# Kernel tuning notes

Hardware: AMD Instinct MI355X
Metric: run time of the kernel (lower is better)

Reference implementation:

```python
import jax, jax.numpy as jnp
import numpy as np

HIDDEN = 4096
N_HEADS = 32
N_KV_HEADS = 8
HEAD_DIM = HIDDEN // N_HEADS  # 128
N_GROUPS = N_HEADS // N_KV_HEADS  # 4
ROPE_THETA = 10000.0


def setup_inputs() -> dict:
    key = jax.random.key(0)
    k1, k2, k3, k4, k5 = jax.random.split(key, 5)
    B, S = 2, 2048
    hidden_states = jax.random.normal(k1, (B, S, HIDDEN), dtype=jnp.float32)
    position_ids = jnp.arange(S, dtype=jnp.int64 if jax.config.jax_enable_x64 else jnp.int32)[None, :]
    scale = 0.02
    Wq = jax.random.normal(k2, (N_HEADS * HEAD_DIM, HIDDEN), dtype=jnp.float32) * scale
    Wk = jax.random.normal(k3, (N_KV_HEADS * HEAD_DIM, HIDDEN), dtype=jnp.float32) * scale
    Wv = jax.random.normal(k4, (N_KV_HEADS * HEAD_DIM, HIDDEN), dtype=jnp.float32) * scale
    Wo = jax.random.normal(k5, (HIDDEN, N_HEADS * HEAD_DIM), dtype=jnp.float32) * scale
    return {"hidden_states": hidden_states, "position_ids": position_ids,
            "Wq": Wq, "Wk": Wk, "Wv": Wv, "Wo": Wo}


def _rope_cos_sin(position_ids, dtype):
    # inv_freq: [HEAD_DIM/2]
    inv_freq = 1.0 / (ROPE_THETA ** (jnp.arange(0, HEAD_DIM, 2, dtype=jnp.float32) / HEAD_DIM))
    freqs = position_ids.astype(jnp.float32)[..., None] * inv_freq  # [1, S, D/2]
    emb = jnp.concatenate([freqs, freqs], axis=-1)                  # [1, S, D]
    return jnp.cos(emb).astype(dtype), jnp.sin(emb).astype(dtype)


def _rotate_half(x):
    x1, x2 = jnp.split(x, 2, axis=-1)
    return jnp.concatenate([-x2, x1], axis=-1)


def reference(hidden_states, position_ids, Wq, Wk, Wv, Wo):
    B, S, H = hidden_states.shape
    d = HEAD_DIM
    # projections -> [B, heads, S, d]
    q = (hidden_states @ Wq.T).reshape(B, S, N_HEADS, d).transpose(0, 2, 1, 3)
    k = (hidden_states @ Wk.T).reshape(B, S, N_KV_HEADS, d).transpose(0, 2, 1, 3)
    v = (hidden_states @ Wv.T).reshape(B, S, N_KV_HEADS, d).transpose(0, 2, 1, 3)
    cos, sin = _rope_cos_sin(position_ids, q.dtype)  # [1, S, d]
    cos, sin = cos[:, None], sin[:, None]            # [1, 1, S, d]
    q = q * cos + _rotate_half(q) * sin
    k = k * cos + _rotate_half(k) * sin
    # GQA: group query heads over shared kv heads (no explicit expand)
    qg = q.reshape(B, N_KV_HEADS, N_GROUPS, S, d)
    scores = jnp.einsum('bkgqd,bkld->bkgql', qg, k) / jnp.sqrt(jnp.asarray(d, q.dtype))
    w = jax.nn.softmax(scores, axis=-1)  # NOTE: no causal mask, matching source
    o = jnp.einsum('bkgql,bkld->bkgqd', w, v)        # [B, kvh, g, S, d]
    o = o.reshape(B, N_HEADS, S, d).transpose(0, 2, 1, 3).reshape(B, S, N_HEADS * d)
    return o @ Wo.T
```

## Files before the change

kernel.cpp:

```cpp
#include <hip/hip_runtime.h>
#include <math.h>

#define HIDDEN 4096
#define NH 32
#define NKV 8
#define HD 128
#define BBATCH 2
#define SEQ 2048
#define BS 4096
#define QKVD 6144

typedef __attribute__((ext_vector_type(8))) short short8;
typedef __attribute__((ext_vector_type(4))) float f32x4;
typedef __attribute__((ext_vector_type(4))) unsigned int uint4v;

__device__ __forceinline__ unsigned short f2bf(float f) {
  union { float f; unsigned int u; } v; v.f = f;
  unsigned int r = v.u + 0x7fffu + ((v.u >> 16) & 1u);
  return (unsigned short)(r >> 16);
}
__device__ __forceinline__ float bf2f(unsigned short u) {
  union { unsigned int u; float f; } v; v.u = ((unsigned int)u) << 16;
  return v.f;
}
__device__ __forceinline__ unsigned int cvtpk(float lo, float hi) {
  unsigned int r;
  asm("v_cvt_pk_bf16_f32 %0, %1, %2" : "=v"(r) : "v"(lo), "v"(hi));
  return r;
}

__device__ __forceinline__ void gload16(const unsigned short* g, unsigned short* l) {
  __builtin_amdgcn_global_load_lds((const __attribute__((address_space(1))) unsigned int*)(const void*)g,
                                   (__attribute__((address_space(3))) unsigned int*)(void*)l, 16, 0, 0);
}

__global__ void cast_all(const float* __restrict__ h, const float* __restrict__ q,
                         const float* __restrict__ k, const float* __restrict__ v,
                         const float* __restrict__ o,
                         unsigned short* hx, unsigned short* wq, unsigned short* wk,
                         unsigned short* wv, unsigned short* wo) {
  int b = blockIdx.x;
  const float* src; unsigned short* dst; int base;
  if (b < 16384)      { src = h; dst = hx; base = 0; }
  else if (b < 32768) { src = q; dst = wq; base = 16384; }
  else if (b < 36864) { src = k; dst = wk; base = 32768; }
  else if (b < 40960) { src = v; dst = wv; base = 36864; }
  else                { src = o; dst = wo; base = 40960; }
  size_t i = ((size_t)(b - base) * 256 + threadIdx.x) * 4;
  float4 f = *(const float4*)(src + i);
  ushort4 u;
  u.x = f2bf(f.x); u.y = f2bf(f.y); u.z = f2bf(f.z); u.w = f2bf(f.w);
  *(ushort4*)(dst + i) = u;
}

template<int OUT_F32>
__global__ __launch_bounds__(256) void gemm_bt128(const unsigned short* __restrict__ A,
                                                  const unsigned short* __restrict__ Bm,
                                                  void* __restrict__ Cc,
                                                  int M, int N, int K) {
  __shared__ unsigned short As[128 * 32];
  __shared__ unsigned short Bs[128 * 32];
  int t = threadIdx.x, lane = t & 63, wave = t >> 6;
  int lm = lane & 15, quad = lane >> 4;
  int wm = wave >> 1, wn = wave & 1;
  int m0 = blockIdx.y * 128, n0 = blockIdx.x * 128;
  int srow = t >> 2;
  int pcol = (((t & 3) ^ (srow & 3)) * 8);
  f32x4 acc[4][4] = {};
  const unsigned short* ag = A + (size_t)(m0 + srow) * K + pcol;
  const unsigned short* bg = Bm + (size_t)(n0 + srow) * K + pcol;
  unsigned short* asl = &As[(size_t)t * 8];
  unsigned short* bsl = &Bs[(size_t)t * 8];
  for (int k0 = 0; k0 < K; k0 += 32) {
    __syncthreads();
    gload16(ag + k0, asl);
    gload16(ag + (size_t)64 * K + k0, asl + 2048);
    gload16(bg + k0, bsl);
    gload16(bg + (size_t)64 * K + k0, bsl + 2048);
    __syncthreads();
    int xq = (quad ^ (lm & 3)) * 8;
    short8 af[4], bf[4];
#pragma unroll
    for (int mt = 0; mt < 4; mt++)
      af[mt] = *(const short8*)&As[(wm * 64 + mt * 16 + lm) * 32 + xq];
#pragma unroll
    for (int nt = 0; nt < 4; nt++)
      bf[nt] = *(const short8*)&Bs[(wn * 64 + nt * 16 + lm) * 32 + xq];
#pragma unroll
    for (int mt = 0; mt < 4; mt++)
#pragma unroll
      for (int nt = 0; nt < 4; nt++)
        acc[mt][nt] = __builtin_amdgcn_mfma_f32_16x16x32_bf16(af[mt], bf[nt], acc[mt][nt], 0, 0, 0);
  }
#pragma unroll
  for (int mt = 0; mt < 4; mt++)
#pragma unroll
    for (int nt = 0; nt < 4; nt++)
#pragma unroll
      for (int r = 0; r < 4; r++) {
        size_t row = m0 + wm * 64 + mt * 16 + quad * 4 + r;
        size_t col = n0 + wn * 64 + nt * 16 + lm;
        if (OUT_F32) ((float*)Cc)[row * N + col] = acc[mt][nt][r];
        else ((unsigned short*)Cc)[row * N + col] = f2bf(acc[mt][nt][r]);
      }
}

__global__ void build_rope_table(const int* __restrict__ pos, float2* __restrict__ cs) {
  int idx = blockIdx.x * blockDim.x + threadIdx.x;
  int j = idx & 63, s = idx >> 6;
  float p = (float)pos[s];
  float f = p * exp2f(-(float)j * (13.287712379549449f / 64.0f));
  cs[idx] = make_float2(cosf(f), sinf(f));
}

__global__ void rope_fused(unsigned short* __restrict__ x, const float2* __restrict__ cs) {
  int idx = blockIdx.x * blockDim.x + threadIdx.x;
  int j = idx & 63;
  int q6 = idx >> 6;
  int hh = q6 % 40;
  int row = q6 / 40;
  int s = row & (SEQ - 1);
  float2 t2 = cs[(s << 6) | j];
  unsigned short* ptr = x + (size_t)row * QKVD + hh * HD;
  float x1 = bf2f(ptr[j]), x2 = bf2f(ptr[j + 64]);
  ptr[j]      = f2bf(x1 * t2.x - x2 * t2.y);
  ptr[j + 64] = f2bf(x2 * t2.x + x1 * t2.y);
}

__global__ void transpose_v(const unsigned short* __restrict__ v, unsigned short* __restrict__ vt) {
  __shared__ unsigned short tile[64][72];
  int bx = blockIdx.x;
  int s0 = (bx & 31) * 64;
  int d0 = ((bx >> 5) & 1) * 64;
  int bk = bx >> 6;
  int b = bk >> 3, kv = bk & 7;
  int t = threadIdx.x;
  int rs = t >> 2, rc = (t & 3) * 16;
  const unsigned short* src = v + ((size_t)(b * SEQ + s0 + rs)) * QKVD + kv * HD + d0 + rc;
  *(uint4*)&tile[rs][rc]     = *(const uint4*)src;
  *(uint4*)&tile[rs][rc + 8] = *(const uint4*)(src + 8);
  __syncthreads();
  int wd = t >> 2, wc = (t & 3) * 16;
  short8 o0, o1;
#pragma unroll
  for (int e = 0; e < 8; e++) o0[e] = (short)tile[wc + e][wd];
#pragma unroll
  for (int e = 0; e < 8; e++) o1[e] = (short)tile[wc + 8 + e][wd];
  unsigned short* dst = vt + ((size_t)bk * HD + d0 + wd) * SEQ + s0 + wc;
  *(short8*)dst = o0;
  *(short8*)(dst + 8) = o1;
}

__global__ __launch_bounds__(256) void attn_kernel(const unsigned short* __restrict__ Q,
                                                   const unsigned short* __restrict__ Kb,
                                                   const unsigned short* __restrict__ Vt,
                                                   unsigned short* __restrict__ O) {
  __shared__ unsigned short Ksh[2 * 64 * 128];
  __shared__ unsigned short Vsh[2 * 128 * 64];
  int t = threadIdx.x, wave = t >> 6, lane = t & 63;
  int lm = lane & 15, quad = lane >> 4;
  int blk0 = blockIdx.x;
  int blk = (blk0 & 7) * 128 + (blk0 >> 3);
  int qt = blk & 15;
  int h = (blk >> 4) & 31;
  int b = blk >> 9;
  int kv = h >> 2;
  int qs0 = qt * 128 + wave * 32;
  const float c = 0.08838834764831845f * 1.4426950408889634f;

  short8 aq[2][4];
#pragma unroll
  for (int s = 0; s < 2; s++) {
    const unsigned short* qbase = Q + ((size_t)(b * SEQ + qs0 + s * 16 + lm)) * QKVD + h * HD;
#pragma unroll
    for (int kk = 0; kk < 4; kk++)
      aq[s][kk] = *(const short8*)(qbase + kk * 32 + quad * 8);
  }

  f32x4 acc[2][8] = {};
  float mrow[2] = {-1e30f, -1e30f};
  float lrow[2] = {0.f, 0.f};
  const unsigned short* kbase = Kb + (size_t)b * SEQ * QKVD + kv * HD;
  const unsigned short* vbase = Vt + ((size_t)(b * NKV + kv)) * HD * SEQ;

  int trow = t >> 4;
  int kchunk = (t & 15) ^ (trow & 7);
  const unsigned short* ksrc[4];
#pragma unroll
  for (int i = 0; i < 4; i++) {
    int srow = i * 16 + trow;
    int key = (srow & 0x20) | ((srow & 0x0C) << 1) | ((srow & 0x10) >> 2) | (srow & 3);
    ksrc[i] = kbase + (size_t)key * QKVD + kchunk * 8;
  }
  int vrow = t >> 3;
  int vchunk = (t & 7) ^ (vrow & 7);
  const unsigned short* vsrc[4];
#pragma unroll
  for (int i = 0; i < 4; i++)
    vsrc[i] = vbase + (size_t)(i * 32 + vrow) * SEQ + vchunk * 8;

  int xr8 = (lm & 7) * 8;

  {
    unsigned short* kd = Ksh + t * 8;
    unsigned short* vd = Vsh + t * 8;
#pragma unroll
    for (int i = 0; i < 4; i++) gload16(ksrc[i], kd + i * 2048);
#pragma unroll
    for (int i = 0; i < 4; i++) gload16(vsrc[i], vd + i * 2048);
#pragma unroll
    for (int i = 0; i < 4; i++) { ksrc[i] += 64 * QKVD; vsrc[i] += 64; }
  }
  asm volatile("s_waitcnt vmcnt(0)" ::: "memory");
  __syncthreads();

  int cur = 0;
  for (int it = 0; it < SEQ / 64; it++) {
    if (it < SEQ / 64 - 1) {
      unsigned short* kd = Ksh + (cur ^ 1) * 8192 + t * 8;
      unsigned short* vd = Vsh + (cur ^ 1) * 8192 + t * 8;
#pragma unroll
      for (int i = 0; i < 4; i++) gload16(ksrc[i], kd + i * 2048);
#pragma unroll
      for (int i = 0; i < 4; i++) gload16(vsrc[i], vd + i * 2048);
#pragma unroll
      for (int i = 0; i < 4; i++) { ksrc[i] += 64 * QKVD; vsrc[i] += 64; }
    }
    const unsigned short* kcur = Ksh + cur * 8192;
    const unsigned short* vcur = Vsh + cur * 8192;
    f32x4 sc[2][4] = {};
    __builtin_amdgcn_s_setprio(1);
#pragma unroll
    for (int kt = 0; kt < 4; kt++) {
#pragma unroll
      for (int kk = 0; kk < 4; kk++) {
        short8 bk = *(const short8*)&kcur[(kt * 16 + lm) * 128 + (((kk * 4 + quad) * 8) ^ xr8)];
        sc[0][kt] = __builtin_amdgcn_mfma_f32_16x16x32_bf16(bk, aq[0][kk], sc[0][kt], 0, 0, 0);
        sc[1][kt] = __builtin_amdgcn_mfma_f32_16x16x32_bf16(bk, aq[1][kk], sc[1][kt], 0, 0, 0);
      }
    }
    __builtin_amdgcn_s_setprio(0);
    union PW { uint4v w; short8 h; } pw[2][2];
#pragma unroll
    for (int s = 0; s < 2; s++) {
      float vmax = -1e30f;
#pragma unroll
      for (int kt = 0; kt < 4; kt++)
        vmax = fmaxf(vmax, fmaxf(fmaxf(sc[s][kt][0], sc[s][kt][1]),
                                 fmaxf(sc[s][kt][2], sc[s][kt][3])));
      vmax *= c;
      vmax = fmaxf(vmax, __shfl_xor(vmax, 16));
      vmax = fmaxf(vmax, __shfl_xor(vmax, 32));
      if (__any(vmax > mrow[s] + 8.0f)) {
        float nm = fmaxf(mrow[s], vmax);
        float alpha = __builtin_amdgcn_exp2f(mrow[s] - nm);
        mrow[s] = nm;
        lrow[s] *= alpha;
#pragma unroll
        for (int r = 0; r < 4; r++) {
          float ar = __shfl(alpha, quad * 4 + r);
#pragma unroll
          for (int tt = 0; tt < 8; tt++) acc[s][tt][r] *= ar;
        }
      }
      float nm = mrow[s];
      float rs = 0.f;
#pragma unroll
      for (int kt = 0; kt < 4; kt++) {
        float p0 = __builtin_amdgcn_exp2f(sc[s][kt][0] * c - nm);
        float p1 = __builtin_amdgcn_exp2f(sc[s][kt][1] * c - nm);
        float p2 = __builtin_amdgcn_exp2f(sc[s][kt][2] * c - nm);
        float p3 = __builtin_amdgcn_exp2f(sc[s][kt][3] * c - nm);
        rs += (p0 + p1) + (p2 + p3);
        pw[s][kt >> 1].w[(kt & 1) * 2 + 0] = cvtpk(p0, p1);
        pw[s][kt >> 1].w[(kt & 1) * 2 + 1] = cvtpk(p2, p3);
      }
      rs += __shfl_xor(rs, 16);
      rs += __shfl_xor(rs, 32);
      lrow[s] += rs;
    }
    __builtin_amdgcn_s_setprio(1);
#pragma unroll
    for (int g = 0; g < 2; g++) {
      short8 ap0 = pw[0][g].h;
      short8 ap1 = pw[1][g].h;
#pragma unroll
      for (int tt = 0; tt < 8; tt++) {
        short8 bv = *(const short8*)&vcur[(tt * 16 + lm) * 64 + (((g * 4 + quad) * 8) ^ xr8)];
        acc[0][tt] = __builtin_amdgcn_mfma_f32_16x16x32_bf16(ap0, bv, acc[0][tt], 0, 0, 0);
        acc[1][tt] = __builtin_amdgcn_mfma_f32_16x16x32_bf16(ap1, bv, acc[1][tt], 0, 0, 0);
      }
    }
    __builtin_amdgcn_s_setprio(0);
    asm volatile("s_waitcnt vmcnt(0)" ::: "memory");
    __syncthreads();
    cur ^= 1;
  }
#pragma unroll
  for (int s = 0; s < 2; s++) {
#pragma unroll
    for (int r = 0; r < 4; r++) {
      float lq = __shfl(lrow[s], quad * 4 + r);
      float inv = 1.0f / lq;
      int row = qs0 + s * 16 + quad * 4 + r;
      unsigned short* op = O + ((size_t)(b * SEQ + row)) * HIDDEN + h * HD;
#pragma unroll
      for (int tt = 0; tt < 8; tt++)
        op[tt * 16 + lm] = f2bf(acc[s][tt][r] * inv);
    }
  }
}

extern "C" void kernel_launch(void* const* d_in, const int* in_sizes, int n_in,
                              void* d_out, int out_size, void* d_ws, size_t ws_size,
                              hipStream_t stream) {
  const float* hidden = (const float*)d_in[0];
  const int*   pos    = (const int*)d_in[1];
  const float* Wq     = (const float*)d_in[2];
  const float* Wk     = (const float*)d_in[3];
  const float* Wv     = (const float*)d_in[4];
  const float* Wo     = (const float*)d_in[5];

  char* ws = (char*)d_ws;
  unsigned short* hx  = (unsigned short*)ws; ws += (size_t)BS * HIDDEN * 2;
  unsigned short* wq  = (unsigned short*)ws; ws += (size_t)HIDDEN * HIDDEN * 2;
  unsigned short* wk  = (unsigned short*)ws; ws += (size_t)1024 * HIDDEN * 2;
  unsigned short* wv  = (unsigned short*)ws; ws += (size_t)1024 * HIDDEN * 2;
  unsigned short* wo  = (unsigned short*)ws; ws += (size_t)HIDDEN * HIDDEN * 2;
  unsigned short* qkv = (unsigned short*)ws; ws += (size_t)BS * QKVD * 2;
  unsigned short* vt  = (unsigned short*)ws; ws += (size_t)BS * 1024 * 2;
  unsigned short* ob  = (unsigned short*)ws; ws += (size_t)BS * HIDDEN * 2;
  float2*         cs  = (float2*)ws;         ws += (size_t)SEQ * 64 * sizeof(float2);

  build_rope_table<<<512, 256, 0, stream>>>(pos, cs);
  cast_all<<<57344, 256, 0, stream>>>(hidden, Wq, Wk, Wv, Wo, hx, wq, wk, wv, wo);
  gemm_bt128<0><<<dim3(48, 32), 256, 0, stream>>>(hx, wq, qkv, BS, QKVD, HIDDEN);
  rope_fused<<<40960, 256, 0, stream>>>(qkv, cs);
  transpose_v<<<1024, 256, 0, stream>>>(qkv + HIDDEN + 1024, vt);
  attn_kernel<<<1024, 256, 0, stream>>>(qkv, qkv + HIDDEN, vt, ob);
  gemm_bt128<1><<<dim3(32, 32), 256, 0, stream>>>(ob, wo, d_out, BS, HIDDEN, HIDDEN);
}
```

Before: 892.5 us.

## Use 256x256 double-buffered GEMM tiles with XCD-aware block swizzle

Replaces the 128x128, K=32, single-buffered GEMM with a 256x256 tile over K=64 steps. It uses 512 threads, and each wave computes a 128x64 sub-tile. LDS is double-buffered, so the next K slice is fetched while MFMAs run on the current one. Workgroup IDs are remapped so neighbouring tiles land on the same XCD, and s_setprio is raised around the MFMA bursts. The aim is more data reuse per byte loaded and hidden load latency. In exchange, about 128KB of LDS per block limits occupancy to one block per CU, and the QKV grid of 384 blocks fills the CUs unevenly.

After: 819.9 us. 8.1% less time.

```diff
diff --git a/kernel.cpp b/kernel.cpp
--- a/kernel.cpp
+++ b/kernel.cpp
@@ -54,54 +54,88 @@
 }
 
 template<int OUT_F32>
-__global__ __launch_bounds__(256) void gemm_bt128(const unsigned short* __restrict__ A,
-                                                  const unsigned short* __restrict__ Bm,
-                                                  void* __restrict__ Cc,
-                                                  int M, int N, int K) {
-  __shared__ unsigned short As[128 * 32];
-  __shared__ unsigned short Bs[128 * 32];
+__global__ __launch_bounds__(512, 2) void gemm_bt256(const unsigned short* __restrict__ A,
+                                                     const unsigned short* __restrict__ Bm,
+                                                     void* __restrict__ Cc,
+                                                     int M, int N, int K) {
+  __shared__ unsigned short As[2][256 * 64];
+  __shared__ unsigned short Bs[2][256 * 64];
   int t = threadIdx.x, lane = t & 63, wave = t >> 6;
   int lm = lane & 15, quad = lane >> 4;
-  int wm = wave >> 1, wn = wave & 1;
-  int m0 = blockIdx.y * 128, n0 = blockIdx.x * 128;
-  int srow = t >> 2;
-  int pcol = (((t & 3) ^ (srow & 3)) * 8);
-  f32x4 acc[4][4] = {};
-  const unsigned short* ag = A + (size_t)(m0 + srow) * K + pcol;
-  const unsigned short* bg = Bm + (size_t)(n0 + srow) * K + pcol;
-  unsigned short* asl = &As[(size_t)t * 8];
-  unsigned short* bsl = &Bs[(size_t)t * 8];
-  for (int k0 = 0; k0 < K; k0 += 32) {
+  int wm = wave >> 2, wn = wave & 3;
+  int nwg = gridDim.x * gridDim.y;
+  int id = blockIdx.y * gridDim.x + blockIdx.x;
+  int cpx = nwg >> 3;
+  int sw = (id & 7) * cpx + (id >> 3);
+  int bx = sw % gridDim.x, by = sw / gridDim.x;
+  int m0 = by * 256, n0 = bx * 256;
+
+  int srow = t >> 3;
+  int schunk = ((t & 7) ^ (srow & 7)) * 8;
+  const unsigned short* ag = A + (size_t)(m0 + srow) * K + schunk;
+  const unsigned short* bg = Bm + (size_t)(n0 + srow) * K + schunk;
+
+  f32x4 acc[8][4] = {};
+
+#pragma unroll
+  for (int i = 0; i < 4; i++) gload16(ag + (size_t)i * 64 * K, &As[0][i * 4096 + t * 8]);
+#pragma unroll
+  for (int i = 0; i < 4; i++) gload16(bg + (size_t)i * 64 * K, &Bs[0][i * 4096 + t * 8]);
+  asm volatile("s_waitcnt vmcnt(0)" ::: "memory");
+  __syncthreads();
+
+  int cur = 0;
+  for (int k0 = 0; k0 < K; k0 += 64) {
+    if (k0 + 64 < K) {
+#pragma unroll
+      for (int i = 0; i < 4; i++)
+        gload16(ag + (size_t)i * 64 * K + k0 + 64, &As[cur ^ 1][i * 4096 + t * 8]);
+#pragma unroll
+      for (int i = 0; i < 4; i++)
+        gload16(bg + (size_t)i * 64 * K + k0 + 64, &Bs[cur ^ 1][i * 4096 + t * 8]);
+    }
+    short8 bfr[4][2];
+#pragma unroll
+    for (int n = 0; n < 4; n++)
+#pragma unroll
+      for (int ks = 0; ks < 2; ks++)
+        bfr[n][ks] = *(const short8*)&Bs[cur][(wn * 64 + n * 16 + lm) * 64 +
+                                             (((ks * 4 + quad) ^ (lm & 7)) * 8)];
+#pragma unroll
+    for (int mh = 0; mh < 2; mh++) {
+      short8 afr[4][2];
+#pragma unroll
+      for (int m4 = 0; m4 < 4; m4++)
+#pragma unroll
+        for (int ks = 0; ks < 2; ks++)
+          afr[m4][ks] = *(const short8*)&As[cur][(wm * 128 + (mh * 4 + m4) * 16 + lm) * 64 +
+                                                (((ks * 4 + quad) ^ (lm & 7)) * 8)];
+      __builtin_amdgcn_s_setprio(1);
+#pragma unroll
+      for (int m4 = 0; m4 < 4; m4++)
+#pragma unroll
+        for (int n = 0; n < 4; n++)
+#pragma unroll
+          for (int ks = 0; ks < 2; ks++)
+            acc[mh * 4 + m4][n] =
+                __builtin_amdgcn_mfma_f32_16x16x32_bf16(afr[m4][ks], bfr[n][ks],
+                                                        acc[mh * 4 + m4][n], 0, 0, 0);
+      __builtin_amdgcn_s_setprio(0);
+    }
+    asm volatile("s_waitcnt vmcnt(0)" ::: "memory");
     __syncthreads();
-    gload16(ag + k0, asl);
-    gload16(ag + (size_t)64 * K + k0, asl + 2048);
-    gload16(bg + k0, bsl);
-    gload16(bg + (size_t)64 * K + k0, bsl + 2048);
-    __syncthreads();
-    int xq = (quad ^ (lm & 3)) * 8;
-    short8 af[4], bf[4];
-#pragma unroll
-    for (int mt = 0; mt < 4; mt++)
-      af[mt] = *(const short8*)&As[(wm * 64 + mt * 16 + lm) * 32 + xq];
-#pragma unroll
-    for (int nt = 0; nt < 4; nt++)
-      bf[nt] = *(const short8*)&Bs[(wn * 64 + nt * 16 + lm) * 32 + xq];
-#pragma unroll
-    for (int mt = 0; mt < 4; mt++)
-#pragma unroll
-      for (int nt = 0; nt < 4; nt++)
-        acc[mt][nt] = __builtin_amdgcn_mfma_f32_16x16x32_bf16(af[mt], bf[nt], acc[mt][nt], 0, 0, 0);
-  }
-#pragma unroll
-  for (int mt = 0; mt < 4; mt++)
-#pragma unroll
-    for (int nt = 0; nt < 4; nt++)
+    cur ^= 1;
+  }
+#pragma unroll
+  for (int m = 0; m < 8; m++)
+#pragma unroll
+    for (int n = 0; n < 4; n++)
 #pragma unroll
       for (int r = 0; r < 4; r++) {
-        size_t row = m0 + wm * 64 + mt * 16 + quad * 4 + r;
-        size_t col = n0 + wn * 64 + nt * 16 + lm;
-        if (OUT_F32) ((float*)Cc)[row * N + col] = acc[mt][nt][r];
-        else ((unsigned short*)Cc)[row * N + col] = f2bf(acc[mt][nt][r]);
+        size_t row = m0 + wm * 128 + m * 16 + quad * 4 + r;
+        size_t col = n0 + wn * 64 + n * 16 + lm;
+        if (OUT_F32) ((float*)Cc)[row * N + col] = acc[m][n][r];
+        else ((unsigned short*)Cc)[row * N + col] = f2bf(acc[m][n][r]);
       }
 }
 
@@ -334,9 +368,9 @@
 
   build_rope_table<<<512, 256, 0, stream>>>(pos, cs);
   cast_all<<<57344, 256, 0, stream>>>(hidden, Wq, Wk, Wv, Wo, hx, wq, wk, wv, wo);
-  gemm_bt128<0><<<dim3(48, 32), 256, 0, stream>>>(hx, wq, qkv, BS, QKVD, HIDDEN);
+  gemm_bt256<0><<<dim3(24, 16), 512, 0, stream>>>(hx, wq, qkv, BS, QKVD, HIDDEN);
   rope_fused<<<40960, 256, 0, stream>>>(qkv, cs);
   transpose_v<<<1024, 256, 0, stream>>>(qkv + HIDDEN + 1024, vt);
   attn_kernel<<<1024, 256, 0, stream>>>(qkv, qkv + HIDDEN, vt, ob);
-  gemm_bt128<1><<<dim3(32, 32), 256, 0, stream>>>(ob, wo, d_out, BS, HIDDEN, HIDDEN);
-}
+  gemm_bt256<1><<<dim3(16, 16), 512, 0, stream>>>(ob, wo, d_out, BS, HIDDEN, HIDDEN);
+}
```
